# Optimization experiments

Measured on AMD Instinct MI355X. Metric: run time of the kernel, lower is better.

The kernel has to match this reference:

```python
import jax, jax.numpy as jnp
import numpy as np

B, S, D = 32, 256, 512   # batch, seq, shared_base hdim
N, H, O = 16, 256, 2     # num_tasks heads, adapter hidden, output_dim
VOCAB = 1024             # property-token lookup table length


def setup_inputs() -> dict:
    key = jax.random.key(0)
    ks = jax.random.split(key, 10)
    adapter_input = jax.random.normal(ks[0], (B, S, D), dtype=jnp.float32)
    tasks = jax.random.randint(ks[1], (B, S), 0, VOCAB, dtype=jnp.int64)
    lookup_table = jax.random.randint(ks[2], (VOCAB,), 0, N, dtype=jnp.int64)
    s1 = 1.0 / np.sqrt(D)
    s2 = 1.0 / np.sqrt(H)
    W1 = jax.random.uniform(ks[3], (N, D, H), jnp.float32, -s1, s1)
    b1 = jax.random.uniform(ks[4], (N, H), jnp.float32, -s1, s1)
    W2 = jax.random.uniform(ks[5], (N, H, H), jnp.float32, -s2, s2)
    b2 = jax.random.uniform(ks[6], (N, H), jnp.float32, -s2, s2)
    W3 = jax.random.uniform(ks[7], (N, H, O), jnp.float32, -s2, s2)
    b3 = jax.random.uniform(ks[8], (N, O), jnp.float32, -s2, s2)
    return dict(adapter_input=adapter_input, tasks=tasks, lookup_table=lookup_table,
                W1=W1, b1=b1, W2=W2, b2=b2, W3=W3, b3=b3)


def reference(adapter_input, tasks, lookup_table, W1, b1, W2, b2, W3, b3):
    # --- PropertyToIndexRouter: task token -> head index (-1 if out of range / unmapped)
    L = lookup_table.shape[0]
    clamped = jnp.clip(tasks, 0, L - 1)
    head_indices = lookup_table[clamped]
    invalid = (tasks >= L) | (tasks < 0)
    head_indices = jnp.where(invalid, -1, head_indices)          # [B, S]

    valid = head_indices >= 0
    idx = jnp.where(valid, head_indices, 0)                      # safe gather index

    # --- each head's SimpleAdapter run densely over all tokens (dropout=eval no-op),
    # vectorized over the head dim instead of a Python loop per head
    h1 = jax.nn.relu(jnp.einsum('bsd,ndh->bsnh', adapter_input, W1) + b1)   # [B,S,N,H]
    h2 = jax.nn.relu(jnp.einsum('bsnh,nhk->bsnk', h1, W2) + b2)             # [B,S,N,H]
    out_all = jnp.einsum('bsnk,nko->bsno', h2, W3) + b3                     # [B,S,N,O]

    # --- masked scatter-combine: pick each token's assigned head, zeros elsewhere
    out = jnp.take_along_axis(out_all, idx[:, :, None, None], axis=2)[:, :, 0, :]  # [B,S,O]
    out = jnp.where(valid[:, :, None], out, jnp.zeros((), out.dtype))
    return out
```

## Files before the change

### kernel.cpp

```cpp
#include <hip/hip_runtime.h>

#define TOK_TOTAL 8192
#define DDIM 512
#define HDIM 256
#define ODIM 2
#define NHEADS 16
#define VOCAB 1024

typedef __attribute__((ext_vector_type(8))) short short8;
typedef __attribute__((ext_vector_type(4))) float f32x4;
typedef __attribute__((ext_vector_type(4))) unsigned short ushort4v;

__device__ inline ushort f2bf(float f) {
    uint u = __float_as_uint(f);
    uint r = (u + 0x7fffu + ((u >> 16) & 1u)) >> 16;
    return (ushort)r;
}
__device__ inline float bf2f(ushort h) { return __uint_as_float(((uint)h) << 16); }

__global__ __launch_bounds__(256) void mth_prep_route(
    const float* __restrict__ W1, const float* __restrict__ W2,
    const int* __restrict__ tasks, const int* __restrict__ lut,
    ushort* __restrict__ W1h, ushort* __restrict__ W2h,
    int* __restrict__ counts, int* __restrict__ lists,
    float* __restrict__ out)
{
    const int b = blockIdx.x, t = threadIdx.x;

    if (b < 384) {
        __shared__ float s[32][257];
        const float* src;
        ushort* dh;
        if (b < 256) {
            const int n = b >> 4, kc = b & 15;
            src = W1 + (size_t)(n * 16 + kc) * 8192;
            dh  = W1h + (size_t)(n * 16 + kc) * 8192;
        } else {
            const int b2 = b - 256, n = b2 >> 3, kc = b2 & 7;
            src = W2 + (size_t)(n * 8 + kc) * 8192;
            dh  = W2h + (size_t)(n * 8 + kc) * 8192;
        }
        #pragma unroll
        for (int i = 0; i < 8; ++i) {
            const int q = t + i * 256;
            const float4 f = ((const float4*)src)[q];
            const int k = q >> 6, c4 = (q & 63) * 4;
            s[k][c4] = f.x; s[k][c4 + 1] = f.y; s[k][c4 + 2] = f.z; s[k][c4 + 3] = f.w;
        }
        __syncthreads();
        #pragma unroll
        for (int i = 0; i < 4; ++i) {
            const int s8 = t + i * 256;
            const int lidx = s8 & 63;
            const int c = (s8 >> 6) * 16 + (lidx & 15);
            const int kw = (lidx >> 4) * 8;
            short8 hb;
            #pragma unroll
            for (int j = 0; j < 8; ++j) hb[j] = (short)f2bf(s[kw + j][c]);
            *(short8*)(dh + (size_t)s8 * 8) = hb;
        }
        return;
    }

    const int i = b - 384;
    __shared__ int hist[16];
    __shared__ int wcnt[4][16];
    if (t < 16) hist[t] = 0;
    __syncthreads();
    for (int q = t; q < i * 256; q += 256) {
        const int task = tasks[q];
        const int h = (task >= 0 && task < VOCAB) ? lut[task] : -1;
        if (h >= 0) atomicAdd(&hist[h], 1);
    }
    const int tok = i * 256 + t;
    const int task = tasks[tok];
    const int h = (task >= 0 && task < VOCAB) ? lut[task] : -1;
    if (h < 0) {
        out[(size_t)tok * 2]     = 0.f;
        out[(size_t)tok * 2 + 1] = 0.f;
    }
    const int w = t >> 6, l = t & 63;
    const unsigned long long lt = (1ULL << l) - 1ULL;
    int pre = 0;
    #pragma unroll
    for (int n = 0; n < NHEADS; ++n) {
        const unsigned long long m = __ballot(h == n);
        if (h == n) pre = (int)__popcll(m & lt);
        if (l == 0) wcnt[w][n] = (int)__popcll(m);
    }
    __syncthreads();
    if (h >= 0) {
        int off = hist[h];
        for (int w2 = 0; w2 < w; ++w2) off += wcnt[w2][h];
        lists[h * TOK_TOTAL + off + pre] = tok;
    }
    if (i == 31 && t < 16) {
        int tot = hist[t];
        #pragma unroll
        for (int w2 = 0; w2 < 4; ++w2) tot += wcnt[w2][t];
        counts[t] = tot;
    }
}

__global__ __launch_bounds__(512) void mth_mlp7(
    const float* __restrict__ X, const int* __restrict__ counts,
    const int* __restrict__ lists,
    const ushort* __restrict__ W1h, const ushort* __restrict__ W2h,
    const float* __restrict__ b1, const float* __restrict__ b2,
    const float* __restrict__ W3, const float* __restrict__ b3,
    float* __restrict__ out)
{
    __shared__ __align__(16) ushort Ah[16][64][8];
    __shared__ __align__(16) ushort Al[16][64][8];
    __shared__ __align__(16) ushort Hh[8][64][8];
    __shared__ __align__(16) ushort Hl[8][64][8];
    __shared__ float part[8][16][2];

    const int b = blockIdx.x;
    const int n = ((b & 7) << 1) | ((b >> 3) & 1);
    const int tile0 = b >> 4;

    const int tid = threadIdx.x;
    const int w   = tid >> 6;
    const int l   = tid & 63;
    const int r16 = l & 15;
    const int kg  = l >> 4;

    const int cnt = counts[n];
    const int listbase = n * TOK_TOTAL;

    float bias1[2], bias2[2];
    float2 w3v[2];
    #pragma unroll
    for (int cf = 0; cf < 2; ++cf) {
        const int col = w * 32 + cf * 16 + r16;
        bias1[cf] = b1[n * HDIM + col];
        bias2[cf] = b2[n * HDIM + col];
        w3v[cf]   = *(const float2*)(W3 + (size_t)(n * HDIM + col) * 2);
    }
    const ushort* w1hn = W1h + (size_t)n * (16 * 8192);
    const ushort* w2hn = W2h + (size_t)n * (8 * 8192);
    const int le8 = l * 8;

    for (int T = tile0; T * 16 < cnt; T += 32) {
        #pragma unroll
        for (int p = 0; p < 4; ++p) {
            const int q   = tid + p * 512;
            const int row = q >> 7;
            const int f4  = q & 127;
            const int tokidx = min(T * 16 + row, cnt - 1);
            const int tok = lists[listbase + tokidx];
            const float4 f = *(const float4*)(X + (size_t)tok * DDIM + f4 * 4);
            const int kc  = f4 >> 3;
            const int kgw = (f4 >> 1) & 3;
            const int j0  = (f4 & 1) * 4;
            const int ln2 = (kgw * 16 + row) ^ (kc & 7);
            ushort4v hv, lv;
            const float vv[4] = {f.x, f.y, f.z, f.w};
            #pragma unroll
            for (int e = 0; e < 4; ++e) {
                const uint u = __float_as_uint(vv[e]);
                hv[e] = (ushort)(u >> 16);
                lv[e] = f2bf(vv[e] - __uint_as_float(u & 0xffff0000u));
            }
            *(ushort4v*)&Ah[kc][ln2][j0] = hv;
            *(ushort4v*)&Al[kc][ln2][j0] = lv;
        }
        __syncthreads();

        f32x4 acc[2];
        #pragma unroll
        for (int cf = 0; cf < 2; ++cf) acc[cf] = (f32x4){0.f, 0.f, 0.f, 0.f};

        #pragma unroll 4
        for (int kc = 0; kc < 16; ++kc) {
            const int ls = l ^ (kc & 7);
            const short8 ah = *(const short8*)&Ah[kc][ls][0];
            const short8 al = *(const short8*)&Al[kc][ls][0];
            const ushort* bp = w1hn + kc * 8192 + le8;
            #pragma unroll
            for (int cf = 0; cf < 2; ++cf) {
                const short8 bh = *(const short8*)(bp + (w * 2 + cf) * 512);
                acc[cf] = __builtin_amdgcn_mfma_f32_16x16x32_bf16(ah, bh, acc[cf], 0, 0, 0);
                acc[cf] = __builtin_amdgcn_mfma_f32_16x16x32_bf16(al, bh, acc[cf], 0, 0, 0);
            }
        }

        #pragma unroll
        for (int cf = 0; cf < 2; ++cf) {
            const int lp = (cf * 2 + (r16 >> 3)) * 16;
            const int e  = r16 & 7;
            #pragma unroll
            for (int j = 0; j < 4; ++j) {
                const float v = fmaxf(acc[cf][j] + bias1[cf], 0.f);
                const uint u = __float_as_uint(v);
                Hh[w][lp + kg * 4 + j][e] = (ushort)(u >> 16);
                Hl[w][lp + kg * 4 + j][e] =
                    f2bf(v - __uint_as_float(u & 0xffff0000u));
            }
        }
        __syncthreads();

        f32x4 acc2[2];
        #pragma unroll
        for (int cf = 0; cf < 2; ++cf) acc2[cf] = (f32x4){0.f, 0.f, 0.f, 0.f};

        #pragma unroll 4
        for (int kc = 0; kc < 8; ++kc) {
            const short8 ah = *(const short8*)&Hh[kc][l][0];
            const short8 al = *(const short8*)&Hl[kc][l][0];
            const ushort* bp = w2hn + kc * 8192 + le8;
            #pragma unroll
            for (int cf = 0; cf < 2; ++cf) {
                const short8 bh = *(const short8*)(bp + (w * 2 + cf) * 512);
                acc2[cf] = __builtin_amdgcn_mfma_f32_16x16x32_bf16(ah, bh, acc2[cf], 0, 0, 0);
                acc2[cf] = __builtin_amdgcn_mfma_f32_16x16x32_bf16(al, bh, acc2[cf], 0, 0, 0);
            }
        }

        float p[4][2];
        #pragma unroll
        for (int j = 0; j < 4; ++j) { p[j][0] = 0.f; p[j][1] = 0.f; }
        #pragma unroll
        for (int cf = 0; cf < 2; ++cf) {
            #pragma unroll
            for (int j = 0; j < 4; ++j) {
                const float v = fmaxf(acc2[cf][j] + bias2[cf], 0.f);
                p[j][0] = fmaf(v, w3v[cf].x, p[j][0]);
                p[j][1] = fmaf(v, w3v[cf].y, p[j][1]);
            }
        }
        #pragma unroll
        for (int off = 8; off >= 1; off >>= 1) {
            #pragma unroll
            for (int j = 0; j < 4; ++j) {
                p[j][0] += __shfl_xor(p[j][0], off);
                p[j][1] += __shfl_xor(p[j][1], off);
            }
        }
        if (r16 == 0) {
            #pragma unroll
            for (int j = 0; j < 4; ++j) {
                part[w][kg * 4 + j][0] = p[j][0];
                part[w][kg * 4 + j][1] = p[j][1];
            }
        }
        __syncthreads();

        if (tid < 32) {
            const int tk = tid >> 1, o = tid & 1;
            if (T * 16 + tk < cnt) {
                float s = 0.f;
                #pragma unroll
                for (int w2 = 0; w2 < 8; ++w2) s += part[w2][tk][o];
                const int tok = lists[listbase + T * 16 + tk];
                out[(size_t)tok * 2 + o] = s + b3[n * 2 + o];
            }
        }
        __syncthreads();
    }
}

#define CHUNKS 16
#define CHUNK (TOK_TOTAL / CHUNKS)
#define TILE 32
#define KB 16

__global__ __launch_bounds__(256) void mth_routed_fp32(
    const float* __restrict__ X, const int* __restrict__ tasks,
    const int* __restrict__ lut,
    const float* __restrict__ W1, const float* __restrict__ b1,
    const float* __restrict__ W2, const float* __restrict__ b2,
    const float* __restrict__ W3, const float* __restrict__ b3,
    float* __restrict__ out)
{
    const int n = blockIdx.x, chnk = blockIdx.y, tid = threadIdx.x;
    const int lane = tid & 63, wv = tid >> 6, tx = tid & 31, ty = tid >> 5;
    __shared__ int s_list[CHUNK];
    __shared__ int s_cnt[8];
    __shared__ __align__(16) float s_x[KB][TILE];
    __shared__ __align__(16) float s_w[KB][HDIM];
    __shared__ __align__(16) float s_h[HDIM][TILE];
    const int base = chnk * CHUNK;
    int mytok[2], mypre[2], myseg[2]; bool mymatch[2];
    #pragma unroll
    for (int i = 0; i < 2; ++i) {
        const int tok = base + i * 256 + tid;
        const int task = tasks[tok];
        const int hidx = (task >= 0 && task < VOCAB) ? lut[task] : -1;
        const bool match = (hidx == n);
        const unsigned long long mask = __ballot(match);
        mytok[i] = tok; mymatch[i] = match;
        mypre[i] = __popcll(mask & ((1ULL << lane) - 1ULL));
        myseg[i] = i * 4 + wv;
        if (lane == 0) s_cnt[i * 4 + wv] = (int)__popcll(mask);
    }
    __syncthreads();
    int total = 0; int myoff[2] = {0, 0};
    #pragma unroll
    for (int s2 = 0; s2 < 8; ++s2) {
        if (s2 == myseg[0]) myoff[0] = total;
        if (s2 == myseg[1]) myoff[1] = total;
        total += s_cnt[s2];
    }
    #pragma unroll
    for (int i = 0; i < 2; ++i)
        if (mymatch[i]) s_list[myoff[i] + mypre[i]] = mytok[i];
    __syncthreads();
    const int ntok = total;
    if (ntok == 0) return;
    float bias1[8], bias2[8];
    #pragma unroll
    for (int j = 0; j < 8; ++j) {
        bias1[j] = b1[n * HDIM + tx * 8 + j];
        bias2[j] = b2[n * HDIM + tx * 8 + j];
    }
    float w3v[16];
    #pragma unroll
    for (int j = 0; j < 16; ++j) w3v[j] = W3[n * HDIM * ODIM + tx * 8 * ODIM + j];
    const float b3v0 = b3[n * ODIM + 0], b3v1 = b3[n * ODIM + 1];
    const float* W1n = W1 + (size_t)n * DDIM * HDIM;
    const float* W2n = W2 + (size_t)n * HDIM * HDIM;
    for (int ts = 0; ts < ntok; ts += TILE) {
        const int m = min(TILE, ntok - ts);
        float acc[4][8];
        #pragma unroll
        for (int t = 0; t < 4; ++t)
            #pragma unroll
            for (int j = 0; j < 8; ++j) acc[t][j] = 0.f;
        for (int kc = 0; kc < DDIM / KB; ++kc) {
            const float4* src = (const float4*)(W1n + kc * KB * HDIM);
            float4* dst = (float4*)s_w;
            #pragma unroll
            for (int p = 0; p < 4; ++p) dst[tid + p * 256] = src[tid + p * 256];
            #pragma unroll
            for (int p = 0; p < 2; ++p) {
                const int e = tid + p * 256;
                const int dd = e >> 5, t = e & 31;
                float v = 0.f;
                if (t < m) v = X[(size_t)s_list[ts + t] * DDIM + kc * KB + dd];
                s_x[dd][t] = v;
            }
            __syncthreads();
            #pragma unroll
            for (int dd = 0; dd < KB; ++dd) {
                const float4 xa = *(const float4*)&s_x[dd][ty * 4];
                const float4 wa = *(const float4*)&s_w[dd][tx * 8];
                const float4 wb = *(const float4*)&s_w[dd][tx * 8 + 4];
                const float xs[4] = {xa.x, xa.y, xa.z, xa.w};
                const float ws[8] = {wa.x, wa.y, wa.z, wa.w, wb.x, wb.y, wb.z, wb.w};
                #pragma unroll
                for (int t = 0; t < 4; ++t)
                    #pragma unroll
                    for (int j = 0; j < 8; ++j) acc[t][j] = fmaf(xs[t], ws[j], acc[t][j]);
            }
            __syncthreads();
        }
        #pragma unroll
        for (int j = 0; j < 8; ++j) {
            float4 v;
            v.x = fmaxf(acc[0][j] + bias1[j], 0.f);
            v.y = fmaxf(acc[1][j] + bias1[j], 0.f);
            v.z = fmaxf(acc[2][j] + bias1[j], 0.f);
            v.w = fmaxf(acc[3][j] + bias1[j], 0.f);
            *(float4*)&s_h[tx * 8 + j][ty * 4] = v;
        }
        __syncthreads();
        float acc2[4][8];
        #pragma unroll
        for (int t = 0; t < 4; ++t)
            #pragma unroll
            for (int j = 0; j < 8; ++j) acc2[t][j] = 0.f;
        for (int kc = 0; kc < HDIM / KB; ++kc) {
            const float4* src = (const float4*)(W2n + kc * KB * HDIM);
            float4* dst = (float4*)s_w;
            #pragma unroll
            for (int p = 0; p < 4; ++p) dst[tid + p * 256] = src[tid + p * 256];
            __syncthreads();
            #pragma unroll
            for (int dd = 0; dd < KB; ++dd) {
                const int k = kc * KB + dd;
                const float4 xa = *(const float4*)&s_h[k][ty * 4];
                const float4 wa = *(const float4*)&s_w[dd][tx * 8];
                const float4 wb = *(const float4*)&s_w[dd][tx * 8 + 4];
                const float xs[4] = {xa.x, xa.y, xa.z, xa.w};
                const float ws[8] = {wa.x, wa.y, wa.z, wa.w, wb.x, wb.y, wb.z, wb.w};
                #pragma unroll
                for (int t = 0; t < 4; ++t)
                    #pragma unroll
                    for (int j = 0; j < 8; ++j) acc2[t][j] = fmaf(xs[t], ws[j], acc2[t][j]);
            }
            __syncthreads();
        }
        float p0[4] = {0.f, 0.f, 0.f, 0.f}, p1[4] = {0.f, 0.f, 0.f, 0.f};
        #pragma unroll
        for (int t = 0; t < 4; ++t)
            #pragma unroll
            for (int j = 0; j < 8; ++j) {
                const float v = fmaxf(acc2[t][j] + bias2[j], 0.f);
                p0[t] = fmaf(v, w3v[j * 2 + 0], p0[t]);
                p1[t] = fmaf(v, w3v[j * 2 + 1], p1[t]);
            }
        #pragma unroll
        for (int off = 16; off > 0; off >>= 1)
            #pragma unroll
            for (int t = 0; t < 4; ++t) {
                p0[t] += __shfl_xor(p0[t], off);
                p1[t] += __shfl_xor(p1[t], off);
            }
        if (tx == 0) {
            #pragma unroll
            for (int t = 0; t < 4; ++t) {
                const int ti = ty * 4 + t;
                if (ti < m) {
                    const int tok = s_list[ts + ti];
                    out[tok * ODIM + 0] = p0[t] + b3v0;
                    out[tok * ODIM + 1] = p1[t] + b3v1;
                }
            }
        }
        __syncthreads();
    }
}

extern "C" void kernel_launch(void* const* d_in, const int* in_sizes, int n_in,
                              void* d_out, int out_size, void* d_ws, size_t ws_size,
                              hipStream_t stream) {
    (void)in_sizes; (void)n_in;
    const float* X     = (const float*)d_in[0];
    const int*   tasks = (const int*)d_in[1];
    const int*   lut   = (const int*)d_in[2];
    const float* W1    = (const float*)d_in[3];
    const float* b1    = (const float*)d_in[4];
    const float* W2    = (const float*)d_in[5];
    const float* b2    = (const float*)d_in[6];
    const float* W3    = (const float*)d_in[7];
    const float* b3    = (const float*)d_in[8];
    float* out = (float*)d_out;

    const size_t OFF_COUNTS = 0;
    const size_t OFF_LISTS  = 64;
    const size_t OFF_W1H    = OFF_LISTS + (size_t)NHEADS * TOK_TOTAL * 4;
    const size_t NW1        = (size_t)NHEADS * DDIM * HDIM;
    const size_t NW2        = (size_t)NHEADS * HDIM * HDIM;
    const size_t OFF_W2H    = OFF_W1H + NW1 * 2;
    const size_t NEED       = OFF_W2H + NW2 * 2;

    if (ws_size < NEED) {
        hipMemsetAsync(out, 0, (size_t)out_size * sizeof(float), stream);
        dim3 grid(NHEADS, CHUNKS);
        mth_routed_fp32<<<grid, 256, 0, stream>>>(X, tasks, lut, W1, b1, W2, b2, W3, b3, out);
        return;
    }

    char* ws = (char*)d_ws;
    int*    counts = (int*)(ws + OFF_COUNTS);
    int*    lists  = (int*)(ws + OFF_LISTS);
    ushort* W1h    = (ushort*)(ws + OFF_W1H);
    ushort* W2h    = (ushort*)(ws + OFF_W2H);

    mth_prep_route<<<416, 256, 0, stream>>>(W1, W2, tasks, lut,
                                            W1h, W2h, counts, lists, out);
    mth_mlp7<<<512, 512, 0, stream>>>(X, counts, lists, W1h, W2h,
                                      b1, b2, W3, b3, out);
}
```

Baseline: 37.26 us.

## Process 32-token tiles per block and drop low-part split for X input

```diff
diff --git a/kernel.cpp b/kernel.cpp
--- a/kernel.cpp
+++ b/kernel.cpp
@@ -102,7 +102,7 @@
     }
 }
 
-__global__ __launch_bounds__(512) void mth_mlp7(
+__global__ __launch_bounds__(512) void mth_mlp8(
     const float* __restrict__ X, const int* __restrict__ counts,
     const int* __restrict__ lists,
     const ushort* __restrict__ W1h, const ushort* __restrict__ W2h,
@@ -110,11 +110,10 @@
     const float* __restrict__ W3, const float* __restrict__ b3,
     float* __restrict__ out)
 {
-    __shared__ __align__(16) ushort Ah[16][64][8];
-    __shared__ __align__(16) ushort Al[16][64][8];
-    __shared__ __align__(16) ushort Hh[8][64][8];
-    __shared__ __align__(16) ushort Hl[8][64][8];
-    __shared__ float part[8][16][2];
+    __shared__ __align__(16) ushort Ah[16][2][64][8];
+    __shared__ __align__(16) ushort Hh[8][2][64][8];
+    __shared__ __align__(16) ushort Hl[8][2][64][8];
+    __shared__ float part[8][32][2];
 
     const int b = blockIdx.x;
     const int n = ((b & 7) << 1) | ((b >> 3) & 1);
@@ -142,118 +141,135 @@
     const ushort* w2hn = W2h + (size_t)n * (8 * 8192);
     const int le8 = l * 8;
 
-    for (int T = tile0; T * 16 < cnt; T += 32) {
-        #pragma unroll
-        for (int p = 0; p < 4; ++p) {
+    for (int T = tile0; T * 32 < cnt; T += 16) {
+        #pragma unroll
+        for (int p = 0; p < 8; ++p) {
             const int q   = tid + p * 512;
             const int row = q >> 7;
             const int f4  = q & 127;
-            const int tokidx = min(T * 16 + row, cnt - 1);
+            const int tokidx = min(T * 32 + row, cnt - 1);
             const int tok = lists[listbase + tokidx];
             const float4 f = *(const float4*)(X + (size_t)tok * DDIM + f4 * 4);
             const int kc  = f4 >> 3;
             const int kgw = (f4 >> 1) & 3;
             const int j0  = (f4 & 1) * 4;
-            const int ln2 = (kgw * 16 + row) ^ (kc & 7);
-            ushort4v hv, lv;
+            const int tfs = row >> 4;
+            const int rs  = row & 15;
+            const int ln2 = (kgw * 16 + rs) ^ (kc & 7);
+            ushort4v hv;
             const float vv[4] = {f.x, f.y, f.z, f.w};
             #pragma unroll
-            for (int e = 0; e < 4; ++e) {
-                const uint u = __float_as_uint(vv[e]);
-                hv[e] = (ushort)(u >> 16);
-                lv[e] = f2bf(vv[e] - __uint_as_float(u & 0xffff0000u));
-            }
-            *(ushort4v*)&Ah[kc][ln2][j0] = hv;
-            *(ushort4v*)&Al[kc][ln2][j0] = lv;
-        }
-        __syncthreads();
-
-        f32x4 acc[2];
-        #pragma unroll
-        for (int cf = 0; cf < 2; ++cf) acc[cf] = (f32x4){0.f, 0.f, 0.f, 0.f};
+            for (int e = 0; e < 4; ++e) hv[e] = f2bf(vv[e]);
+            *(ushort4v*)&Ah[kc][tfs][ln2][j0] = hv;
+        }
+        __syncthreads();
+
+        f32x4 acc[2][2];
+        #pragma unroll
+        for (int tf = 0; tf < 2; ++tf)
+            #pragma unroll
+            for (int cf = 0; cf < 2; ++cf) acc[tf][cf] = (f32x4){0.f, 0.f, 0.f, 0.f};
 
         #pragma unroll 4
         for (int kc = 0; kc < 16; ++kc) {
             const int ls = l ^ (kc & 7);
-            const short8 ah = *(const short8*)&Ah[kc][ls][0];
-            const short8 al = *(const short8*)&Al[kc][ls][0];
+            const short8 ah0 = *(const short8*)&Ah[kc][0][ls][0];
+            const short8 ah1 = *(const short8*)&Ah[kc][1][ls][0];
             const ushort* bp = w1hn + kc * 8192 + le8;
             #pragma unroll
             for (int cf = 0; cf < 2; ++cf) {
                 const short8 bh = *(const short8*)(bp + (w * 2 + cf) * 512);
-                acc[cf] = __builtin_amdgcn_mfma_f32_16x16x32_bf16(ah, bh, acc[cf], 0, 0, 0);
-                acc[cf] = __builtin_amdgcn_mfma_f32_16x16x32_bf16(al, bh, acc[cf], 0, 0, 0);
-            }
-        }
-
-        #pragma unroll
-        for (int cf = 0; cf < 2; ++cf) {
-            const int lp = (cf * 2 + (r16 >> 3)) * 16;
-            const int e  = r16 & 7;
-            #pragma unroll
-            for (int j = 0; j < 4; ++j) {
-                const float v = fmaxf(acc[cf][j] + bias1[cf], 0.f);
-                const uint u = __float_as_uint(v);
-                Hh[w][lp + kg * 4 + j][e] = (ushort)(u >> 16);
-                Hl[w][lp + kg * 4 + j][e] =
-                    f2bf(v - __uint_as_float(u & 0xffff0000u));
-            }
-        }
-        __syncthreads();
-
-        f32x4 acc2[2];
-        #pragma unroll
-        for (int cf = 0; cf < 2; ++cf) acc2[cf] = (f32x4){0.f, 0.f, 0.f, 0.f};
+                acc[0][cf] = __builtin_amdgcn_mfma_f32_16x16x32_bf16(ah0, bh, acc[0][cf], 0, 0, 0);
+                acc[1][cf] = __builtin_amdgcn_mfma_f32_16x16x32_bf16(ah1, bh, acc[1][cf], 0, 0, 0);
+            }
+        }
+
+        #pragma unroll
+        for (int tf = 0; tf < 2; ++tf) {
+            #pragma unroll
+            for (int cf = 0; cf < 2; ++cf) {
+                const int lp = (cf * 2 + (r16 >> 3)) * 16;
+                const int e  = r16 & 7;
+                #pragma unroll
+                for (int j = 0; j < 4; ++j) {
+                    const float v = fmaxf(acc[tf][cf][j] + bias1[cf], 0.f);
+                    const uint u = __float_as_uint(v);
+                    Hh[w][tf][lp + kg * 4 + j][e] = (ushort)(u >> 16);
+                    Hl[w][tf][lp + kg * 4 + j][e] =
+                        f2bf(v - __uint_as_float(u & 0xffff0000u));
+                }
+            }
+        }
+        __syncthreads();
+
+        f32x4 acc2[2][2];
+        #pragma unroll
+        for (int tf = 0; tf < 2; ++tf)
+            #pragma unroll
+            for (int cf = 0; cf < 2; ++cf) acc2[tf][cf] = (f32x4){0.f, 0.f, 0.f, 0.f};
 
         #pragma unroll 4
         for (int kc = 0; kc < 8; ++kc) {
-            const short8 ah = *(const short8*)&Hh[kc][l][0];
-            const short8 al = *(const short8*)&Hl[kc][l][0];
+            const short8 ah0 = *(const short8*)&Hh[kc][0][l][0];
+            const short8 al0 = *(const short8*)&Hl[kc][0][l][0];
+            const short8 ah1 = *(const short8*)&Hh[kc][1][l][0];
+            const short8 al1 = *(const short8*)&Hl[kc][1][l][0];
             const ushort* bp = w2hn + kc * 8192 + le8;
             #pragma unroll
             for (int cf = 0; cf < 2; ++cf) {
                 const short8 bh = *(const short8*)(bp + (w * 2 + cf) * 512);
-                acc2[cf] = __builtin_amdgcn_mfma_f32_16x16x32_bf16(ah, bh, acc2[cf], 0, 0, 0);
-                acc2[cf] = __builtin_amdgcn_mfma_f32_16x16x32_bf16(al, bh, acc2[cf], 0, 0, 0);
-            }
-        }
-
-        float p[4][2];
-        #pragma unroll
-        for (int j = 0; j < 4; ++j) { p[j][0] = 0.f; p[j][1] = 0.f; }
-        #pragma unroll
-        for (int cf = 0; cf < 2; ++cf) {
-            #pragma unroll
-            for (int j = 0; j < 4; ++j) {
-                const float v = fmaxf(acc2[cf][j] + bias2[cf], 0.f);
-                p[j][0] = fmaf(v, w3v[cf].x, p[j][0]);
-                p[j][1] = fmaf(v, w3v[cf].y, p[j][1]);
+                acc2[0][cf] = __builtin_amdgcn_mfma_f32_16x16x32_bf16(ah0, bh, acc2[0][cf], 0, 0, 0);
+                acc2[0][cf] = __builtin_amdgcn_mfma_f32_16x16x32_bf16(al0, bh, acc2[0][cf], 0, 0, 0);
+                acc2[1][cf] = __builtin_amdgcn_mfma_f32_16x16x32_bf16(ah1, bh, acc2[1][cf], 0, 0, 0);
+                acc2[1][cf] = __builtin_amdgcn_mfma_f32_16x16x32_bf16(al1, bh, acc2[1][cf], 0, 0, 0);
+            }
+        }
+
+        float p[2][4][2];
+        #pragma unroll
+        for (int tf = 0; tf < 2; ++tf)
+            #pragma unroll
+            for (int j = 0; j < 4; ++j) { p[tf][j][0] = 0.f; p[tf][j][1] = 0.f; }
+        #pragma unroll
+        for (int tf = 0; tf < 2; ++tf) {
+            #pragma unroll
+            for (int cf = 0; cf < 2; ++cf) {
+                #pragma unroll
+                for (int j = 0; j < 4; ++j) {
+                    const float v = fmaxf(acc2[tf][cf][j] + bias2[cf], 0.f);
+                    p[tf][j][0] = fmaf(v, w3v[cf].x, p[tf][j][0]);
+                    p[tf][j][1] = fmaf(v, w3v[cf].y, p[tf][j][1]);
+                }
             }
         }
         #pragma unroll
         for (int off = 8; off >= 1; off >>= 1) {
             #pragma unroll
-            for (int j = 0; j < 4; ++j) {
-                p[j][0] += __shfl_xor(p[j][0], off);
-                p[j][1] += __shfl_xor(p[j][1], off);
-            }
+            for (int tf = 0; tf < 2; ++tf)
+                #pragma unroll
+                for (int j = 0; j < 4; ++j) {
+                    p[tf][j][0] += __shfl_xor(p[tf][j][0], off);
+                    p[tf][j][1] += __shfl_xor(p[tf][j][1], off);
+                }
         }
         if (r16 == 0) {
             #pragma unroll
-            for (int j = 0; j < 4; ++j) {
-                part[w][kg * 4 + j][0] = p[j][0];
-                part[w][kg * 4 + j][1] = p[j][1];
-            }
-        }
-        __syncthreads();
-
-        if (tid < 32) {
+            for (int tf = 0; tf < 2; ++tf)
+                #pragma unroll
+                for (int j = 0; j < 4; ++j) {
+                    part[w][tf * 16 + kg * 4 + j][0] = p[tf][j][0];
+                    part[w][tf * 16 + kg * 4 + j][1] = p[tf][j][1];
+                }
+        }
+        __syncthreads();
+
+        if (tid < 64) {
             const int tk = tid >> 1, o = tid & 1;
-            if (T * 16 + tk < cnt) {
+            if (T * 32 + tk < cnt) {
                 float s = 0.f;
                 #pragma unroll
                 for (int w2 = 0; w2 < 8; ++w2) s += part[w2][tk][o];
-                const int tok = lists[listbase + T * 16 + tk];
+                const int tok = lists[listbase + T * 32 + tk];
                 out[(size_t)tok * 2 + o] = s + b3[n * 2 + o];
             }
         }
@@ -461,6 +477,6 @@
 
     mth_prep_route<<<416, 256, 0, stream>>>(W1, W2, tasks, lut,
                                             W1h, W2h, counts, lists, out);
-    mth_mlp7<<<512, 512, 0, stream>>>(X, counts, lists, W1h, W2h,
+    mth_mlp8<<<256, 512, 0, stream>>>(X, counts, lists, W1h, W2h,
                                       b1, b2, W3, b3, out);
 }
```

Measured after the change: 39.77 us. 6.8% more time.
